# Kernel tuning notes

Measured on AMD Instinct MI355X. Metric: run time of the kernel, lower is better.

Reference implementation:

```python
import jax, jax.numpy as jnp
import numpy as np

B, S, E = 4, 2048, 768
H = 12
D = E // H  # 64

def setup_inputs() -> dict:
    key = jax.random.key(0)
    k_x, k_wqkv, k_wproj = jax.random.split(key, 3)
    x = jax.random.normal(k_x, (B, S, E), dtype=jnp.float32)
    w_qkv = jax.random.normal(k_wqkv, (E, 3 * E), dtype=jnp.float32) * 0.02
    b_qkv = jnp.zeros((3 * E,), dtype=jnp.float32)
    w_proj = jax.random.normal(k_wproj, (E, E), dtype=jnp.float32) * 0.02
    b_proj = jnp.zeros((E,), dtype=jnp.float32)
    return {"x": x, "w_qkv": w_qkv, "b_qkv": b_qkv, "w_proj": w_proj, "b_proj": b_proj}

def reference(x, w_qkv, b_qkv, w_proj, b_proj):
    # fused QKV projection: [B,S,E] -> [B,S,3E]
    qkv = jnp.einsum("bse,ef->bsf", x, w_qkv) + b_qkv
    qkv = qkv.reshape(B, S, 3, H, D)
    q, k, v = qkv[:, :, 0], qkv[:, :, 1], qkv[:, :, 2]  # [B,S,H,D]
    scale = 1.0 / jnp.sqrt(jnp.asarray(D, dtype=x.dtype))
    # causal scaled dot-product attention (explicit score matrix, as in module)
    scores = jnp.einsum("bshd,bthd->bhst", q, k) * scale  # [B,H,S,S]
    causal = jnp.tril(jnp.ones((S, S), dtype=bool))
    scores = jnp.where(causal, scores, jnp.finfo(scores.dtype).min)
    probs = jax.nn.softmax(scores, axis=-1)
    attn = jnp.einsum("bhst,bthd->bshd", probs, v).reshape(B, S, E)
    # output projection
    out = jnp.einsum("bse,ef->bsf", attn, w_proj) + b_proj
    return out
```

## Files before the change

kernel.cpp:

```cpp
#include <hip/hip_runtime.h>

#define SDIM 2048
#define EDIM 768
#define HDIM 12
#define DDIM 64
#define BDIM 4
#define MROWS (BDIM * SDIM)
#define NQKV (3 * EDIM)
#define NBH (BDIM * HDIM)
#define NTILE 32
#define NPAIR 16

typedef __attribute__((ext_vector_type(8))) short s16x8;
typedef __attribute__((ext_vector_type(4))) float f32x4;
typedef __attribute__((ext_vector_type(2))) unsigned int u32x2;

__device__ __forceinline__ short f2b(float x) {
  union { float f; unsigned u; } v; v.f = x;
  unsigned r = v.u + 0x7fffu + ((v.u >> 16) & 1u);
  return (short)(r >> 16);
}

__device__ __forceinline__ unsigned cvtpk(float lo, float hi) {
  unsigned r;
  asm volatile("v_cvt_pk_bf16_f32 %0, %1, %2" : "=v"(r) : "v"(lo), "v"(hi));
  return r;
}

__device__ __forceinline__ float fexp2(float x) {
  float r;
  asm("v_exp_f32 %0, %1" : "=v"(r) : "v"(x));
  return r;
}

__device__ __forceinline__ void gld16(const void* g, void* l) {
  __builtin_amdgcn_global_load_lds(
      (const __attribute__((address_space(1))) unsigned int*)g,
      (__attribute__((address_space(3))) unsigned int*)l, 16, 0, 0);
}

__global__ __launch_bounds__(256) void preproc(
    const float* __restrict__ x, const float* __restrict__ wqkv,
    const float* __restrict__ wproj, short* __restrict__ xb,
    short* __restrict__ wqkvt, short* __restrict__ wprojt) {
  int bid = blockIdx.x;
  if (bid < 1536) {
    int i = bid * 256 + threadIdx.x;
    const int n4 = MROWS * EDIM / 4;
    for (; i < n4; i += 1536 * 256) {
      float4 v = ((const float4*)x)[i];
      short4 o;
      o.x = f2b(v.x); o.y = f2b(v.y); o.z = f2b(v.z); o.w = f2b(v.w);
      ((short4*)xb)[i] = o;
    }
    return;
  }
  const float* in; short* out; int K, N, t;
  if (bid < 1536 + 1728) { t = bid - 1536; in = wqkv; out = wqkvt; K = EDIM; N = NQKV; }
  else { t = bid - 1536 - 1728; in = wproj; out = wprojt; K = EDIM; N = EDIM; }
  const int ntx = N / 32;
  int n0 = (t % ntx) * 32, k0 = (t / ntx) * 32;
  __shared__ float tb[32][33];
  int tx = threadIdx.x & 31, ty = threadIdx.x >> 5;
#pragma unroll
  for (int i = 0; i < 4; ++i)
    tb[ty + 8 * i][tx] = in[(size_t)(k0 + ty + 8 * i) * N + n0 + tx];
  __syncthreads();
#pragma unroll
  for (int i = 0; i < 4; ++i)
    out[(size_t)(n0 + ty + 8 * i) * K + k0 + tx] = f2b(tb[tx][ty + 8 * i]);
}

__global__ __launch_bounds__(256) void gemm_bf16(
    const short* __restrict__ A, const short* __restrict__ Bt,
    const float* __restrict__ bias, int M, int N, int K, int mode,
    short* __restrict__ qout, short* __restrict__ kout,
    short* __restrict__ vout, float* __restrict__ fout) {
  __shared__ char lds[3][16384];
  const int tid = threadIdx.x;
  const int l = tid & 63, w = tid >> 6;
  const int lr = l & 15, g = l >> 4;

  const int chunk = gridDim.x >> 3;
  const int sid = (blockIdx.x & 7) * chunk + (blockIdx.x >> 3);
  const int ntx = N >> 7;
  const int bm = (sid / ntx) * 128, bn = (sid % ntx) * 128;
  const int wm = w >> 1, wn = w & 1;

  const int srow = w * 32 + (l >> 2);
  const int sc8 = (((l & 3) ^ ((l >> 3) & 3)) << 3);
  const short* Ap0 = A + (size_t)(bm + srow) * K + sc8;
  const short* Bp0 = Bt + (size_t)(bn + srow) * K + sc8;

  f32x4 acc[4][4];
  const f32x4 z4 = {0.f, 0.f, 0.f, 0.f};
#pragma unroll
  for (int m = 0; m < 4; ++m)
#pragma unroll
    for (int n = 0; n < 4; ++n) acc[m][n] = z4;

#define STAGE(dst, t)                          \
  {                                            \
    char* Ad = (dst) + w * 2048;               \
    const short* Ap = Ap0 + (t) * 32;          \
    const short* Bp = Bp0 + (t) * 32;          \
    gld16(Ap, Ad);                             \
    gld16(Ap + 16 * K, Ad + 1024);             \
    gld16(Bp, Ad + 8192);                      \
    gld16(Bp + 16 * K, Ad + 9216);             \
  }

  const int nt = K >> 5;
  STAGE(lds[0], 0);
  STAGE(lds[1], 1);
  asm volatile("s_waitcnt vmcnt(4)" ::: "memory");
  __builtin_amdgcn_s_barrier();

  const int swz = ((lr >> 1) & 3) << 4;
  int bc = 0;
  for (int t = 0; t < nt; ++t) {
    if (t + 2 < nt) {
      int bs = bc + 2; if (bs >= 3) bs -= 3;
      STAGE(lds[bs], t + 2);
    }
    const char* Ab = lds[bc];
    const char* Bb = lds[bc] + 8192;
    s16x8 af[4], bfr[4];
#pragma unroll
    for (int m = 0; m < 4; ++m)
      af[m] = *(const s16x8*)(Ab + (wm * 64 + m * 16 + lr) * 64 + ((g << 4) ^ swz));
#pragma unroll
    for (int n = 0; n < 4; ++n)
      bfr[n] = *(const s16x8*)(Bb + (wn * 64 + n * 16 + lr) * 64 + ((g << 4) ^ swz));
    __builtin_amdgcn_s_setprio(1);
#pragma unroll
    for (int m = 0; m < 4; ++m)
#pragma unroll
      for (int n = 0; n < 4; ++n)
        acc[m][n] = __builtin_amdgcn_mfma_f32_16x16x32_bf16(af[m], bfr[n],
                                                            acc[m][n], 0, 0, 0);
    __builtin_amdgcn_s_setprio(0);
    if (t + 2 < nt) {
      asm volatile("s_waitcnt vmcnt(4)" ::: "memory");
      __builtin_amdgcn_s_barrier();
    } else if (t + 1 < nt) {
      asm volatile("s_waitcnt vmcnt(0)" ::: "memory");
      __builtin_amdgcn_s_barrier();
    }
    if (++bc == 3) bc = 0;
  }
#undef STAGE

#pragma unroll
  for (int m = 0; m < 4; ++m) {
    int rbase = bm + wm * 64 + m * 16 + g * 4;
#pragma unroll
    for (int n = 0; n < 4; ++n) {
      int col = bn + wn * 64 + n * 16 + lr;
      float bv = bias[col];
      if (mode == 0) {
        int which = (col >= 1536) ? 2 : (col >= 768 ? 1 : 0);
        int rem = col - which * 768;
        int h = rem >> 6, d = rem & 63;
#pragma unroll
        for (int i = 0; i < 4; ++i) {
          int r = rbase + i;
          int b = r >> 11, s = r & 2047;
          short o = f2b(acc[m][n][i] + bv);
          size_t bh = (size_t)b * HDIM + h;
          if (which == 0)      qout[(bh * SDIM + s) * DDIM + d] = o;
          else if (which == 1) kout[(bh * SDIM + s) * DDIM + d] = o;
          else                 vout[(bh * DDIM + d) * SDIM + s] = o;
        }
      } else {
#pragma unroll
        for (int i = 0; i < 4; ++i)
          fout[(size_t)(rbase + i) * N + col] = acc[m][n][i] + bv;
      }
    }
  }
}

__global__ __launch_bounds__(256) void attn_mfma3(
    const short* __restrict__ qb, const short* __restrict__ kb,
    const short* __restrict__ vb, short* __restrict__ ao) {
  __shared__ short kvbuf[2][8192];
  __shared__ short pstrip[4][1024];

  const int tid = threadIdx.x;
  const int l = tid & 63, w = tid >> 6;
  const int lr = l & 15, g = l >> 4;
  const int swz = (lr & 7) << 4;

  const int lin = blockIdx.x;
  const int xcd = lin & 7;
  const int idx = lin >> 3;
  const int bh = xcd * 6 + (idx >> 4);
  const int pair = idx & 15;
  const int tiles[2] = {NTILE - 1 - pair, pair};

  const int b = bh / HDIM, h = bh % HDIM;
  const size_t base = (size_t)bh * SDIM * DDIM;

  const int srow = w * 16 + (l >> 3);
  const int sc = (l & 7) ^ (srow & 7);
  const size_t koff0 = (size_t)srow * DDIM + sc * 8;
  const size_t koff1 = (size_t)(srow + 8) * DDIM + sc * 8;
  const size_t voff0 = (size_t)srow * SDIM + sc * 8;
  const size_t voff1 = (size_t)(srow + 8) * SDIM + sc * 8;

  const float SC = 0.125f * 1.4426950408889634f;
  char* sw = (char*)pstrip[w];

  for (int half = 0; half < 2; ++half) {
    const int tile = tiles[half];
    const int q0w = tile * 64 + w * 16;

    s16x8 qa[2];
#pragma unroll
    for (int s = 0; s < 2; ++s)
      qa[s] = *(const s16x8*)(qb + base + (size_t)(q0w + lr) * DDIM + s * 32 + g * 8);

    const f32x4 z4 = {0.f, 0.f, 0.f, 0.f};
    f32x4 acco[4];
#pragma unroll
    for (int nd = 0; nd < 4; ++nd) acco[nd] = z4;
    float mrun = -1e30f, lsum = 0.f;

    int cur = 0;
    {
      char* kd = (char*)kvbuf[cur] + w * 2048;
      const short* kp = kb + base;
      const short* vp = vb + base;
      gld16(kp + koff0, kd);
      gld16(kp + koff1, kd + 1024);
      gld16(vp + voff0, kd + 8192);
      gld16(vp + voff1, kd + 9216);
    }
    __syncthreads();

    for (int kt = 0; kt <= tile; ++kt) {
      if (kt < tile) {
        char* kd = (char*)kvbuf[cur ^ 1] + w * 2048;
        const short* kp = kb + base + (size_t)(kt + 1) * 64 * DDIM;
        const short* vp = vb + base + (size_t)(kt + 1) * 64;
        gld16(kp + koff0, kd);
        gld16(kp + koff1, kd + 1024);
        gld16(vp + voff0, kd + 8192);
        gld16(vp + voff1, kd + 9216);
      }

      const char* Kb = (const char*)kvbuf[cur];
      const char* Vb = Kb + 8192;

      f32x4 sacc[4];
#pragma unroll
      for (int nt = 0; nt < 4; ++nt) sacc[nt] = z4;
      __builtin_amdgcn_s_setprio(1);
#pragma unroll
      for (int s = 0; s < 2; ++s)
#pragma unroll
        for (int nt = 0; nt < 4; ++nt) {
          s16x8 kf = *(const s16x8*)(Kb + nt * 2048 + lr * 128 +
                                     ((s * 64 + g * 16) ^ swz));
          sacc[nt] = __builtin_amdgcn_mfma_f32_16x16x32_bf16(kf, qa[s],
                                                             sacc[nt], 0, 0, 0);
        }
      __builtin_amdgcn_s_setprio(0);

      if (kt == tile) {
        const int rloc = w * 16 + lr;
#pragma unroll
        for (int nt = 0; nt < 4; ++nt)
#pragma unroll
          for (int i = 0; i < 4; ++i)
            if (nt * 16 + g * 4 + i > rloc) sacc[nt][i] = -1e30f;
      }

      float t0 = fmaxf(fmaxf(sacc[0][0], sacc[0][1]), fmaxf(sacc[0][2], sacc[0][3]));
      float t1 = fmaxf(fmaxf(sacc[1][0], sacc[1][1]), fmaxf(sacc[1][2], sacc[1][3]));
      float t2 = fmaxf(fmaxf(sacc[2][0], sacc[2][1]), fmaxf(sacc[2][2], sacc[2][3]));
      float t3 = fmaxf(fmaxf(sacc[3][0], sacc[3][1]), fmaxf(sacc[3][2], sacc[3][3]));
      float pmax = fmaxf(fmaxf(t0, t1), fmaxf(t2, t3));
      pmax = fmaxf(pmax, __shfl_xor(pmax, 16, 64));
      pmax = fmaxf(pmax, __shfl_xor(pmax, 32, 64));

      if (__any(pmax > mrun + 44.0f)) {
        float nm = fmaxf(mrun, pmax);
        float al = fexp2((mrun - nm) * SC);
        lsum *= al;
#pragma unroll
        for (int nd = 0; nd < 4; ++nd)
#pragma unroll
          for (int i = 0; i < 4; ++i) acco[nd][i] *= al;
        mrun = nm;
      }

      const float msc = mrun * SC;
#pragma unroll
      for (int nt = 0; nt < 4; ++nt) {
        float p0 = fexp2(__builtin_fmaf(sacc[nt][0], SC, -msc));
        float p1 = fexp2(__builtin_fmaf(sacc[nt][1], SC, -msc));
        float p2 = fexp2(__builtin_fmaf(sacc[nt][2], SC, -msc));
        float p3 = fexp2(__builtin_fmaf(sacc[nt][3], SC, -msc));
        lsum += (p0 + p1) + (p2 + p3);
        u32x2 pk = {cvtpk(p0, p1), cvtpk(p2, p3)};
        *(u32x2*)(sw + lr * 128 + (((nt * 32 + g * 8) ^ swz))) = pk;
      }

      __builtin_amdgcn_s_setprio(1);
#pragma unroll
      for (int s = 0; s < 2; ++s) {
        s16x8 pf = *(const s16x8*)(sw + lr * 128 + ((s * 64 + g * 16) ^ swz));
#pragma unroll
        for (int nd = 0; nd < 4; ++nd) {
          s16x8 vf = *(const s16x8*)(Vb + nd * 2048 + lr * 128 +
                                     ((s * 64 + g * 16) ^ swz));
          acco[nd] = __builtin_amdgcn_mfma_f32_16x16x32_bf16(vf, pf,
                                                             acco[nd], 0, 0, 0);
        }
      }
      __builtin_amdgcn_s_setprio(0);

      __syncthreads();
      cur ^= 1;
    }

    lsum += __shfl_xor(lsum, 16, 64);
    lsum += __shfl_xor(lsum, 32, 64);
    float inv = 1.0f / lsum;
    size_t orow = ((size_t)b * SDIM + q0w + lr) * EDIM + h * DDIM;
#pragma unroll
    for (int nd = 0; nd < 4; ++nd) {
      unsigned lo = cvtpk(acco[nd][0] * inv, acco[nd][1] * inv);
      unsigned hi = cvtpk(acco[nd][2] * inv, acco[nd][3] * inv);
      *(unsigned*)(ao + orow + nd * 16 + g * 4) = lo;
      *(unsigned*)(ao + orow + nd * 16 + g * 4 + 2) = hi;
    }
  }
}

extern "C" void kernel_launch(void* const* d_in, const int* in_sizes, int n_in,
                              void* d_out, int out_size, void* d_ws,
                              size_t ws_size, hipStream_t stream) {
  const float* x = (const float*)d_in[0];
  const float* w_qkv = (const float*)d_in[1];
  const float* b_qkv = (const float*)d_in[2];
  const float* w_proj = (const float*)d_in[3];
  const float* b_proj = (const float*)d_in[4];
  float* out = (float*)d_out;

  char* p = (char*)d_ws;
  short* xb = (short*)p;      p += (size_t)MROWS * EDIM * 2;
  short* wqkvt = (short*)p;   p += (size_t)NQKV * EDIM * 2;
  short* wprojt = (short*)p;  p += (size_t)EDIM * EDIM * 2;
  short* qbuf = (short*)p;    p += (size_t)NBH * SDIM * DDIM * 2;
  short* kbuf = (short*)p;    p += (size_t)NBH * SDIM * DDIM * 2;
  short* vbuf = (short*)p;    p += (size_t)NBH * SDIM * DDIM * 2;
  short* aob = (short*)p;     p += (size_t)MROWS * EDIM * 2;

  dim3 blk(256);
  preproc<<<dim3(1536 + 1728 + 576), blk, 0, stream>>>(x, w_qkv, w_proj, xb,
                                                       wqkvt, wprojt);
  gemm_bf16<<<dim3((NQKV / 128) * (MROWS / 128)), blk, 0, stream>>>(
      xb, wqkvt, b_qkv, MROWS, NQKV, EDIM, 0, qbuf, kbuf, vbuf, nullptr);
  attn_mfma3<<<dim3(NPAIR * NBH), blk, 0, stream>>>(qbuf, kbuf, vbuf, aob);
  gemm_bf16<<<dim3((EDIM / 128) * (MROWS / 128)), blk, 0, stream>>>(
      aob, wprojt, b_proj, MROWS, EDIM, EDIM, 1, nullptr, nullptr, nullptr, out);
}
```

Measured before the change: 140.0 us.

## Retile bf16 GEMM to 256x256 blocks with 512 threads and 4-stage LDS ring

The QKV and output-projection GEMMs move from 128x128 tiles with 4 waves to 256x256 tiles with 8 waves. Each wave now computes a 128x64 sub-tile with 32 accumulators, which raises reuse of each LDS fragment. The LDS ring grows to four 32KB stages, and the barrier moves to the top of the loop before prefetching stage s+2. The cost is far fewer blocks: 288 for QKV and 96 for the projection on a 256-CU part, plus one block per CU from the 128KB LDS, so load balance and latency hiding may suffer.

```diff
diff --git a/kernel.cpp b/kernel.cpp
--- a/kernel.cpp
+++ b/kernel.cpp
@@ -71,92 +71,84 @@
     out[(size_t)(n0 + ty + 8 * i) * K + k0 + tx] = f2b(tb[tx][ty + 8 * i]);
 }
 
-__global__ __launch_bounds__(256) void gemm_bf16(
+__global__ __launch_bounds__(512, 1) void gemm_bf16(
     const short* __restrict__ A, const short* __restrict__ Bt,
     const float* __restrict__ bias, int M, int N, int K, int mode,
     short* __restrict__ qout, short* __restrict__ kout,
     short* __restrict__ vout, float* __restrict__ fout) {
-  __shared__ char lds[3][16384];
+  __shared__ char lds[4][32768];
   const int tid = threadIdx.x;
   const int l = tid & 63, w = tid >> 6;
   const int lr = l & 15, g = l >> 4;
-
   const int chunk = gridDim.x >> 3;
   const int sid = (blockIdx.x & 7) * chunk + (blockIdx.x >> 3);
-  const int ntx = N >> 7;
-  const int bm = (sid / ntx) * 128, bn = (sid % ntx) * 128;
-  const int wm = w >> 1, wn = w & 1;
+  const int ntx = N >> 8;
+  const int bm = (sid / ntx) << 8, bn = (sid % ntx) << 8;
+  const int wm = w >> 2, wn = w & 3;
 
   const int srow = w * 32 + (l >> 2);
-  const int sc8 = (((l & 3) ^ ((l >> 3) & 3)) << 3);
-  const short* Ap0 = A + (size_t)(bm + srow) * K + sc8;
-  const short* Bp0 = Bt + (size_t)(bn + srow) * K + sc8;
-
-  f32x4 acc[4][4];
+  const int sck = (((l & 3) ^ ((l >> 3) & 3)) << 3);
+  const short* ApG = A + (size_t)(bm + srow) * K + sck;
+  const short* ApG2 = ApG + 16 * K;
+  const short* BpG = Bt + (size_t)(bn + srow) * K + sck;
+  const short* BpG2 = BpG + 16 * K;
+
+  const int rswz = ((lr >> 1) & 3) << 4;
+  const int aoff = (wm * 128 + lr) * 64 + ((g << 4) ^ rswz);
+  const int boff = 16384 + (wn * 64 + lr) * 64 + ((g << 4) ^ rswz);
+
+  f32x4 acc[8][4];
   const f32x4 z4 = {0.f, 0.f, 0.f, 0.f};
 #pragma unroll
-  for (int m = 0; m < 4; ++m)
-#pragma unroll
-    for (int n = 0; n < 4; ++n) acc[m][n] = z4;
-
-#define STAGE(dst, t)                          \
-  {                                            \
-    char* Ad = (dst) + w * 2048;               \
-    const short* Ap = Ap0 + (t) * 32;          \
-    const short* Bp = Bp0 + (t) * 32;          \
-    gld16(Ap, Ad);                             \
-    gld16(Ap + 16 * K, Ad + 1024);             \
-    gld16(Bp, Ad + 8192);                      \
-    gld16(Bp + 16 * K, Ad + 9216);             \
-  }
-
-  const int nt = K >> 5;
-  STAGE(lds[0], 0);
-  STAGE(lds[1], 1);
-  asm volatile("s_waitcnt vmcnt(4)" ::: "memory");
-  __builtin_amdgcn_s_barrier();
-
-  const int swz = ((lr >> 1) & 3) << 4;
-  int bc = 0;
-  for (int t = 0; t < nt; ++t) {
-    if (t + 2 < nt) {
-      int bs = bc + 2; if (bs >= 3) bs -= 3;
-      STAGE(lds[bs], t + 2);
-    }
-    const char* Ab = lds[bc];
-    const char* Bb = lds[bc] + 8192;
-    s16x8 af[4], bfr[4];
-#pragma unroll
-    for (int m = 0; m < 4; ++m)
-      af[m] = *(const s16x8*)(Ab + (wm * 64 + m * 16 + lr) * 64 + ((g << 4) ^ swz));
-#pragma unroll
-    for (int n = 0; n < 4; ++n)
-      bfr[n] = *(const s16x8*)(Bb + (wn * 64 + n * 16 + lr) * 64 + ((g << 4) ^ swz));
+  for (int mf = 0; mf < 8; ++mf)
+#pragma unroll
+    for (int nf = 0; nf < 4; ++nf) acc[mf][nf] = z4;
+
+#define STAGE(s_)                                         \
+  {                                                       \
+    char* d_ = &lds[(s_) & 3][0] + w * 2048;              \
+    const int ko_ = (s_) << 5;                            \
+    gld16(ApG + ko_, d_);                                 \
+    gld16(ApG2 + ko_, d_ + 1024);                         \
+    gld16(BpG + ko_, d_ + 16384);                         \
+    gld16(BpG2 + ko_, d_ + 16384 + 1024);                 \
+  }
+
+  const int NS = K >> 5;
+  STAGE(0);
+  STAGE(1);
+  for (int s = 0; s < NS; ++s) {
+    if (s + 1 < NS) asm volatile("s_waitcnt vmcnt(4)" ::: "memory");
+    else            asm volatile("s_waitcnt vmcnt(0)" ::: "memory");
+    __builtin_amdgcn_s_barrier();
+    asm volatile("" ::: "memory");
+    __builtin_amdgcn_sched_barrier(0);
+    if (s + 2 < NS) STAGE(s + 2);
+    const char* buf = &lds[s & 3][0];
+    s16x8 af[8], bf[4];
+#pragma unroll
+    for (int mf = 0; mf < 8; ++mf)
+      af[mf] = *(const s16x8*)(buf + aoff + mf * 1024);
+#pragma unroll
+    for (int nf = 0; nf < 4; ++nf)
+      bf[nf] = *(const s16x8*)(buf + boff + nf * 1024);
     __builtin_amdgcn_s_setprio(1);
 #pragma unroll
-    for (int m = 0; m < 4; ++m)
-#pragma unroll
-      for (int n = 0; n < 4; ++n)
-        acc[m][n] = __builtin_amdgcn_mfma_f32_16x16x32_bf16(af[m], bfr[n],
-                                                            acc[m][n], 0, 0, 0);
+    for (int mf = 0; mf < 8; ++mf)
+#pragma unroll
+      for (int nf = 0; nf < 4; ++nf)
+        acc[mf][nf] = __builtin_amdgcn_mfma_f32_16x16x32_bf16(af[mf], bf[nf],
+                                                              acc[mf][nf], 0, 0, 0);
     __builtin_amdgcn_s_setprio(0);
-    if (t + 2 < nt) {
-      asm volatile("s_waitcnt vmcnt(4)" ::: "memory");
-      __builtin_amdgcn_s_barrier();
-    } else if (t + 1 < nt) {
-      asm volatile("s_waitcnt vmcnt(0)" ::: "memory");
-      __builtin_amdgcn_s_barrier();
-    }
-    if (++bc == 3) bc = 0;
   }
 #undef STAGE
 
 #pragma unroll
-  for (int m = 0; m < 4; ++m) {
-    int rbase = bm + wm * 64 + m * 16 + g * 4;
-#pragma unroll
-    for (int n = 0; n < 4; ++n) {
-      int col = bn + wn * 64 + n * 16 + lr;
+  for (int mf = 0; mf < 8; ++mf) {
+    int rbase = bm + wm * 128 + mf * 16 + g * 4;
+#pragma unroll
+    for (int nf = 0; nf < 4; ++nf) {
+      int col = bn + wn * 64 + nf * 16 + lr;
       float bv = bias[col];
       if (mode == 0) {
         int which = (col >= 1536) ? 2 : (col >= 768 ? 1 : 0);
@@ -165,17 +157,17 @@
 #pragma unroll
         for (int i = 0; i < 4; ++i) {
           int r = rbase + i;
-          int b = r >> 11, s = r & 2047;
-          short o = f2b(acc[m][n][i] + bv);
-          size_t bh = (size_t)b * HDIM + h;
-          if (which == 0)      qout[(bh * SDIM + s) * DDIM + d] = o;
-          else if (which == 1) kout[(bh * SDIM + s) * DDIM + d] = o;
-          else                 vout[(bh * DDIM + d) * SDIM + s] = o;
+          int bb = r >> 11, srw = r & 2047;
+          short o = f2b(acc[mf][nf][i] + bv);
+          size_t bh = (size_t)bb * HDIM + h;
+          if (which == 0)      qout[(bh * SDIM + srw) * DDIM + d] = o;
+          else if (which == 1) kout[(bh * SDIM + srw) * DDIM + d] = o;
+          else                 vout[(bh * DDIM + d) * SDIM + srw] = o;
         }
       } else {
 #pragma unroll
         for (int i = 0; i < 4; ++i)
-          fout[(size_t)(rbase + i) * N + col] = acc[m][n][i] + bv;
+          fout[(size_t)(rbase + i) * N + col] = acc[mf][nf][i] + bv;
       }
     }
   }
@@ -362,9 +354,9 @@
   dim3 blk(256);
   preproc<<<dim3(1536 + 1728 + 576), blk, 0, stream>>>(x, w_qkv, w_proj, xb,
                                                        wqkvt, wprojt);
-  gemm_bf16<<<dim3((NQKV / 128) * (MROWS / 128)), blk, 0, stream>>>(
+  gemm_bf16<<<dim3((MROWS / 256) * (NQKV / 256)), dim3(512), 0, stream>>>(
       xb, wqkvt, b_qkv, MROWS, NQKV, EDIM, 0, qbuf, kbuf, vbuf, nullptr);
   attn_mfma3<<<dim3(NPAIR * NBH), blk, 0, stream>>>(qbuf, kbuf, vbuf, aob);
-  gemm_bf16<<<dim3((EDIM / 128) * (MROWS / 128)), blk, 0, stream>>>(
+  gemm_bf16<<<dim3((MROWS / 256) * (EDIM / 256)), dim3(512), 0, stream>>>(
       aob, wprojt, b_proj, MROWS, EDIM, EDIM, 1, nullptr, nullptr, nullptr, out);
 }
```

After: 169.0 us. 20.7% more time.

## Split GEMM into specialized kernels and restructure attention KV prefetch pipeline

Applied to the files above, without the earlier changes.

The generic GEMM is split into a QKV kernel with compile-time dimensions and a projection kernel, removing the runtime mode branch. The attention kernel now issues two KV tiles up front and waits with vmcnt counters and raw barriers instead of __syncthreads, refilling a buffer right after it has been consumed. It also adds a launch-bounds occupancy hint of 3 blocks per CU. The aim is to overlap global loads with MFMA work more fully, at the cost of fragile hand-managed wait counts and possible register pressure from the occupancy hint.

```diff
diff --git a/kernel.cpp b/kernel.cpp
--- a/kernel.cpp
+++ b/kernel.cpp
@@ -71,19 +71,19 @@
     out[(size_t)(n0 + ty + 8 * i) * K + k0 + tx] = f2b(tb[tx][ty + 8 * i]);
 }
 
-__global__ __launch_bounds__(256) void gemm_bf16(
+__global__ __launch_bounds__(256) void gemm_qkv(
     const short* __restrict__ A, const short* __restrict__ Bt,
-    const float* __restrict__ bias, int M, int N, int K, int mode,
-    short* __restrict__ qout, short* __restrict__ kout,
-    short* __restrict__ vout, float* __restrict__ fout) {
+    const float* __restrict__ bias, short* __restrict__ qout,
+    short* __restrict__ kout, short* __restrict__ vout) {
   __shared__ char lds[3][16384];
   const int tid = threadIdx.x;
   const int l = tid & 63, w = tid >> 6;
   const int lr = l & 15, g = l >> 4;
+  const int K = EDIM;
 
   const int chunk = gridDim.x >> 3;
   const int sid = (blockIdx.x & 7) * chunk + (blockIdx.x >> 3);
-  const int ntx = N >> 7;
+  const int ntx = NQKV >> 7;
   const int bm = (sid / ntx) * 128, bn = (sid % ntx) * 128;
   const int wm = w >> 1, wn = w & 1;
 
@@ -158,30 +158,117 @@
     for (int n = 0; n < 4; ++n) {
       int col = bn + wn * 64 + n * 16 + lr;
       float bv = bias[col];
-      if (mode == 0) {
-        int which = (col >= 1536) ? 2 : (col >= 768 ? 1 : 0);
-        int rem = col - which * 768;
-        int h = rem >> 6, d = rem & 63;
-#pragma unroll
-        for (int i = 0; i < 4; ++i) {
-          int r = rbase + i;
-          int b = r >> 11, s = r & 2047;
-          short o = f2b(acc[m][n][i] + bv);
-          size_t bh = (size_t)b * HDIM + h;
-          if (which == 0)      qout[(bh * SDIM + s) * DDIM + d] = o;
-          else if (which == 1) kout[(bh * SDIM + s) * DDIM + d] = o;
-          else                 vout[(bh * DDIM + d) * SDIM + s] = o;
-        }
-      } else {
-#pragma unroll
-        for (int i = 0; i < 4; ++i)
-          fout[(size_t)(rbase + i) * N + col] = acc[m][n][i] + bv;
+      int which = (col >= 1536) ? 2 : (col >= 768 ? 1 : 0);
+      int rem = col - which * 768;
+      int h = rem >> 6, d = rem & 63;
+#pragma unroll
+      for (int i = 0; i < 4; ++i) {
+        int r = rbase + i;
+        int bb = r >> 11, s = r & 2047;
+        short o = f2b(acc[m][n][i] + bv);
+        size_t bh = (size_t)bb * HDIM + h;
+        if (which == 0)      qout[(bh * SDIM + s) * DDIM + d] = o;
+        else if (which == 1) kout[(bh * SDIM + s) * DDIM + d] = o;
+        else                 vout[(bh * DDIM + d) * SDIM + s] = o;
       }
     }
   }
 }
 
-__global__ __launch_bounds__(256) void attn_mfma3(
+__global__ __launch_bounds__(256) void gemm_proj(
+    const short* __restrict__ A, const short* __restrict__ Bt,
+    const float* __restrict__ bias, int M, int N, int K,
+    float* __restrict__ fout) {
+  __shared__ char lds[3][16384];
+  const int tid = threadIdx.x;
+  const int l = tid & 63, w = tid >> 6;
+  const int lr = l & 15, g = l >> 4;
+
+  const int chunk = gridDim.x >> 3;
+  const int sid = (blockIdx.x & 7) * chunk + (blockIdx.x >> 3);
+  const int ntx = N >> 7;
+  const int bm = (sid / ntx) * 128, bn = (sid % ntx) * 128;
+  const int wm = w >> 1, wn = w & 1;
+
+  const int srow = w * 32 + (l >> 2);
+  const int sc8 = (((l & 3) ^ ((l >> 3) & 3)) << 3);
+  const short* Ap0 = A + (size_t)(bm + srow) * K + sc8;
+  const short* Bp0 = Bt + (size_t)(bn + srow) * K + sc8;
+
+  f32x4 acc[4][4];
+  const f32x4 z4 = {0.f, 0.f, 0.f, 0.f};
+#pragma unroll
+  for (int m = 0; m < 4; ++m)
+#pragma unroll
+    for (int n = 0; n < 4; ++n) acc[m][n] = z4;
+
+#define STAGE(dst, t)                          \
+  {                                            \
+    char* Ad = (dst) + w * 2048;               \
+    const short* Ap = Ap0 + (t) * 32;          \
+    const short* Bp = Bp0 + (t) * 32;          \
+    gld16(Ap, Ad);                             \
+    gld16(Ap + 16 * K, Ad + 1024);             \
+    gld16(Bp, Ad + 8192);                      \
+    gld16(Bp + 16 * K, Ad + 9216);             \
+  }
+
+  const int nt = K >> 5;
+  STAGE(lds[0], 0);
+  STAGE(lds[1], 1);
+  asm volatile("s_waitcnt vmcnt(4)" ::: "memory");
+  __builtin_amdgcn_s_barrier();
+
+  const int swz = ((lr >> 1) & 3) << 4;
+  int bc = 0;
+  for (int t = 0; t < nt; ++t) {
+    if (t + 2 < nt) {
+      int bs = bc + 2; if (bs >= 3) bs -= 3;
+      STAGE(lds[bs], t + 2);
+    }
+    const char* Ab = lds[bc];
+    const char* Bb = lds[bc] + 8192;
+    s16x8 af[4], bfr[4];
+#pragma unroll
+    for (int m = 0; m < 4; ++m)
+      af[m] = *(const s16x8*)(Ab + (wm * 64 + m * 16 + lr) * 64 + ((g << 4) ^ swz));
+#pragma unroll
+    for (int n = 0; n < 4; ++n)
+      bfr[n] = *(const s16x8*)(Bb + (wn * 64 + n * 16 + lr) * 64 + ((g << 4) ^ swz));
+    __builtin_amdgcn_s_setprio(1);
+#pragma unroll
+    for (int m = 0; m < 4; ++m)
+#pragma unroll
+      for (int n = 0; n < 4; ++n)
+        acc[m][n] = __builtin_amdgcn_mfma_f32_16x16x32_bf16(af[m], bfr[n],
+                                                            acc[m][n], 0, 0, 0);
+    __builtin_amdgcn_s_setprio(0);
+    if (t + 2 < nt) {
+      asm volatile("s_waitcnt vmcnt(4)" ::: "memory");
+      __builtin_amdgcn_s_barrier();
+    } else if (t + 1 < nt) {
+      asm volatile("s_waitcnt vmcnt(0)" ::: "memory");
+      __builtin_amdgcn_s_barrier();
+    }
+    if (++bc == 3) bc = 0;
+  }
+#undef STAGE
+
+#pragma unroll
+  for (int m = 0; m < 4; ++m) {
+    int rbase = bm + wm * 64 + m * 16 + g * 4;
+#pragma unroll
+    for (int n = 0; n < 4; ++n) {
+      int col = bn + wn * 64 + n * 16 + lr;
+      float bv = bias[col];
+#pragma unroll
+      for (int i = 0; i < 4; ++i)
+        fout[(size_t)(rbase + i) * N + col] = acc[m][n][i] + bv;
+    }
+  }
+}
+
+__global__ __launch_bounds__(256, 3) void attn_mfma4(
     const short* __restrict__ qb, const short* __restrict__ kb,
     const short* __restrict__ vb, short* __restrict__ ao) {
   __shared__ short kvbuf[2][8192];
@@ -212,6 +299,17 @@
   const float SC = 0.125f * 1.4426950408889634f;
   char* sw = (char*)pstrip[w];
 
+#define KVSTAGE(buf_, kt_)                                        \
+  {                                                               \
+    char* kd = (char*)kvbuf[buf_] + w * 2048;                     \
+    const short* kp = kb + base + (size_t)(kt_) * 64 * DDIM;      \
+    const short* vp = vb + base + (size_t)(kt_) * 64;             \
+    gld16(kp + koff0, kd);                                        \
+    gld16(kp + koff1, kd + 1024);                                 \
+    gld16(vp + voff0, kd + 8192);                                 \
+    gld16(vp + voff1, kd + 9216);                                 \
+  }
+
   for (int half = 0; half < 2; ++half) {
     const int tile = tiles[half];
     const int q0w = tile * 64 + w * 16;
@@ -227,30 +325,18 @@
     for (int nd = 0; nd < 4; ++nd) acco[nd] = z4;
     float mrun = -1e30f, lsum = 0.f;
 
-    int cur = 0;
+    KVSTAGE(0, 0);
     {
-      char* kd = (char*)kvbuf[cur] + w * 2048;
-      const short* kp = kb + base;
-      const short* vp = vb + base;
-      gld16(kp + koff0, kd);
-      gld16(kp + koff1, kd + 1024);
-      gld16(vp + voff0, kd + 8192);
-      gld16(vp + voff1, kd + 9216);
-    }
-    __syncthreads();
+      const int t1 = (tile >= 1) ? 1 : 0;
+      KVSTAGE(1, t1);
+    }
 
     for (int kt = 0; kt <= tile; ++kt) {
-      if (kt < tile) {
-        char* kd = (char*)kvbuf[cur ^ 1] + w * 2048;
-        const short* kp = kb + base + (size_t)(kt + 1) * 64 * DDIM;
-        const short* vp = vb + base + (size_t)(kt + 1) * 64;
-        gld16(kp + koff0, kd);
-        gld16(kp + koff1, kd + 1024);
-        gld16(vp + voff0, kd + 8192);
-        gld16(vp + voff1, kd + 9216);
-      }
-
-      const char* Kb = (const char*)kvbuf[cur];
+      if (kt < tile) asm volatile("s_waitcnt vmcnt(4)" ::: "memory");
+      else           asm volatile("s_waitcnt vmcnt(0)" ::: "memory");
+      __builtin_amdgcn_s_barrier();
+
+      const char* Kb = (const char*)kvbuf[kt & 1];
       const char* Vb = Kb + 8192;
 
       f32x4 sacc[4];
@@ -322,8 +408,8 @@
       }
       __builtin_amdgcn_s_setprio(0);
 
-      __syncthreads();
-      cur ^= 1;
+      __builtin_amdgcn_s_barrier();
+      if (kt + 2 <= tile) KVSTAGE(kt & 1, kt + 2);
     }
 
     lsum += __shfl_xor(lsum, 16, 64);
@@ -338,6 +424,7 @@
       *(unsigned*)(ao + orow + nd * 16 + g * 4 + 2) = hi;
     }
   }
+#undef KVSTAGE
 }
 
 extern "C" void kernel_launch(void* const* d_in, const int* in_sizes, int n_in,
@@ -362,9 +449,9 @@
   dim3 blk(256);
   preproc<<<dim3(1536 + 1728 + 576), blk, 0, stream>>>(x, w_qkv, w_proj, xb,
                                                        wqkvt, wprojt);
-  gemm_bf16<<<dim3((NQKV / 128) * (MROWS / 128)), blk, 0, stream>>>(
-      xb, wqkvt, b_qkv, MROWS, NQKV, EDIM, 0, qbuf, kbuf, vbuf, nullptr);
-  attn_mfma3<<<dim3(NPAIR * NBH), blk, 0, stream>>>(qbuf, kbuf, vbuf, aob);
-  gemm_bf16<<<dim3((EDIM / 128) * (MROWS / 128)), blk, 0, stream>>>(
-      aob, wprojt, b_proj, MROWS, EDIM, EDIM, 1, nullptr, nullptr, nullptr, out);
-}
+  gemm_qkv<<<dim3((MROWS / 128) * (NQKV / 128)), blk, 0, stream>>>(
+      xb, wqkvt, b_qkv, qbuf, kbuf, vbuf);
+  attn_mfma4<<<dim3(NPAIR * NBH), blk, 0, stream>>>(qbuf, kbuf, vbuf, aob);
+  gemm_proj<<<dim3((MROWS / 128) * (EDIM / 128)), blk, 0, stream>>>(
+      aob, wprojt, b_proj, MROWS, EDIM, EDIM, out);
+}
```

Result: faster. 136.9 us (median of 3 runs) (-2.2%).
